# Performance work log

Measured on AMD Instinct MI355X. Metric: run time of the kernel, lower is better.

The kernel has to match this reference:

```python
import jax, jax.numpy as jnp
import numpy as np

D_IN, D_K, D_V = 768, 128, 768


def setup_inputs() -> dict:
    key = jax.random.key(0)
    ks = jax.random.split(key, 7)
    x = jax.random.normal(ks[0], (4, 2048, D_IN), dtype=jnp.float32)
    s_in = 1.0 / np.sqrt(D_IN)
    Wq = jax.random.uniform(ks[1], (D_IN, D_K), minval=-s_in, maxval=s_in, dtype=jnp.float32)
    bq = jax.random.uniform(ks[2], (D_K,), minval=-s_in, maxval=s_in, dtype=jnp.float32)
    Wk = jax.random.uniform(ks[3], (D_IN, D_K), minval=-s_in, maxval=s_in, dtype=jnp.float32)
    bk = jax.random.uniform(ks[4], (D_K,), minval=-s_in, maxval=s_in, dtype=jnp.float32)
    Wv = jax.random.uniform(ks[5], (D_IN, D_V), minval=-s_in, maxval=s_in, dtype=jnp.float32)
    bv = jax.random.uniform(ks[6], (D_V,), minval=-s_in, maxval=s_in, dtype=jnp.float32)
    return {"x": x, "Wq": Wq, "bq": bq, "Wk": Wk, "bk": bk, "Wv": Wv, "bv": bv}


def reference(x, Wq, bq, Wk, bk, Wv, bv):
    # q,k: [b,t,d_k]; v: [b,t,d_v]
    q = jnp.einsum('bti,ik->btk', x, Wq) + bq
    k = jnp.einsum('bti,ik->btk', x, Wk) + bk
    v = jnp.einsum('bti,iv->btv', x, Wv) + bv
    scale = 1.0 / jnp.sqrt(jnp.asarray(D_K, dtype=jnp.float32))
    scores = jnp.einsum('bqk,btk->bqt', q, k) * scale  # [b,t,t]
    attn = jax.nn.softmax(scores, axis=-1)
    return jnp.einsum('bqt,btv->bqv', attn, v)
```

## Files before the change

kernel.cpp:

```cpp
#include <hip/hip_runtime.h>
#include <stdint.h>

typedef unsigned short u16;
typedef __attribute__((ext_vector_type(8))) short short8;
typedef __attribute__((ext_vector_type(4))) float f32x4;

#define BATCH 4
#define SEQ   2048
#define DIN   768
#define DK    128
#define DV    768
#define MTOT  (BATCH*SEQ)
#define NQKV  1024

__device__ __forceinline__ u16 f2bf(float f) {
  union { float f; uint32_t u; } v; v.f = f;
  uint32_t r = v.u + 0x7FFFu + ((v.u >> 16) & 1u);
  return (u16)(r >> 16);
}

template<int N> __device__ __forceinline__ void wait_vmcnt() {
  if constexpr (N == 0) asm volatile("s_waitcnt vmcnt(0)" ::: "memory");
  else if constexpr (N == 5) asm volatile("s_waitcnt vmcnt(5)" ::: "memory");
  else if constexpr (N == 6) asm volatile("s_waitcnt vmcnt(6)" ::: "memory");
}

#define GLOAD_LDS(SRC, DST) \
  __builtin_amdgcn_global_load_lds( \
      (const __attribute__((address_space(1))) unsigned int*)(SRC), \
      (__attribute__((address_space(3))) unsigned int*)(DST), 16, 0, 0)

__global__ __launch_bounds__(256) void prep(
    const float* __restrict__ x, u16* __restrict__ xb,
    const float* __restrict__ Wq, const float* __restrict__ bq,
    const float* __restrict__ Wk, const float* __restrict__ bk,
    const float* __restrict__ Wv, const float* __restrict__ bv,
    u16* __restrict__ WbT, float* __restrict__ biasP) {
  const float qs = 0.088388347648318447f;
  __shared__ u16 tile[64][72];
  int b = blockIdx.x;
  int tid = threadIdx.x;
  if (b < 6144) {
    int i = (b * 256 + tid) * 4;
    float4 v = *(const float4*)(x + i);
    u16 o[4] = { f2bf(v.x), f2bf(v.y), f2bf(v.z), f2bf(v.w) };
    *(uint2*)(xb + i) = *(const uint2*)o;
    return;
  }
  int bid2 = b - 6144;
  int y   = bid2 / 12;
  int i0  = (bid2 - y * 12) * 64;
  const float* W; u16* dst; int ldw, nb; float sc;
  if (y < 2)      { W = Wq; dst = WbT;                      ldw = DK; sc = qs;   nb = y;     }
  else if (y < 4) { W = Wk; dst = WbT + (size_t)DK * DIN;   ldw = DK; sc = 1.0f; nb = y - 2; }
  else            { W = Wv; dst = WbT + (size_t)2*DK * DIN; ldw = DV; sc = 1.0f; nb = y - 4; }
  int n0 = nb * 64;
  if (i0 == 0 && y == 0) {
    for (int n = tid; n < NQKV; n += 256)
      biasP[n] = (n < DK) ? bq[n] * qs : (n < 2*DK ? bk[n - DK] : bv[n - 2*DK]);
  }
  int tr = tid >> 2;
  int tc = (tid & 3) * 16;
  const float* src = W + (size_t)(i0 + tr) * ldw + n0 + tc;
  u16 o[16];
#pragma unroll
  for (int u = 0; u < 16; u += 4) {
    float4 v = *(const float4*)(src + u);
    o[u] = f2bf(v.x * sc); o[u+1] = f2bf(v.y * sc); o[u+2] = f2bf(v.z * sc); o[u+3] = f2bf(v.w * sc);
  }
  *(uint4*)&tile[tr][tc]     = *(const uint4*)&o[0];
  *(uint4*)&tile[tr][tc + 8] = *(const uint4*)&o[8];
  __syncthreads();
  u16 tmp[16];
#pragma unroll
  for (int u = 0; u < 16; ++u) tmp[u] = tile[tc + u][tr];
  u16* d = dst + (size_t)(n0 + tr) * DIN + i0 + tc;
  *(uint4*)d       = *(const uint4*)&tmp[0];
  *(uint4*)(d + 8) = *(const uint4*)&tmp[8];
}

__global__ __launch_bounds__(512, 2) void gemm_proj(
    const u16* __restrict__ A, const u16* __restrict__ BT,
    u16* __restrict__ C0, u16* __restrict__ C1,
    const float* __restrict__ bias)
{
  const int NT = DIN / 64;
  __shared__ u16 As[3][128][64];
  __shared__ u16 Bs[3][256][64];
  const int tid = threadIdx.x;
  const int l   = tid & 63;
  const int wid = tid >> 6;
  const int wm  = wid >> 2;
  const int wn  = wid & 3;

  const int nwg = gridDim.x;
  const int cpx = nwg >> 3;
  const int bid = blockIdx.x;
  const int wg  = (bid & 7) * cpx + (bid >> 3);
  const int by  = wg >> 6;
  const int bx  = wg & 63;
  const int m0  = bx * 128;
  const int n0  = by * 256;

  f32x4 acc[4][4] = {};
  const int lr = l >> 3;
  const int lc = ((l & 7) ^ lr) * 8;

  auto STAGE = [&](int buf, int k0, int i0r, int i1r) {
#pragma unroll
    for (int i = 0; i < 6; ++i) {
      if (i < i0r || i >= i1r) continue;
      int c = wid * 6 + i;
      if (c < 16) {
        GLOAD_LDS(A + (size_t)(m0 + c * 8 + lr) * DIN + k0 + lc, &As[buf][c * 8][0]);
      } else {
        int cb = c - 16;
        GLOAD_LDS(BT + (size_t)(n0 + cb * 8 + lr) * DIN + k0 + lc, &Bs[buf][cb * 8][0]);
      }
    }
  };

  STAGE(0, 0, 0, 6);
  STAGE(1, 64, 0, 6);
  int cur = 0;
  for (int t = 0; t < NT; ++t) {
    if (t == NT - 1) wait_vmcnt<0>(); else wait_vmcnt<6>();
    __builtin_amdgcn_s_barrier();
    const int nxt2 = (cur + 2 >= 3) ? cur - 1 : cur + 2;
    const bool pf = (t + 2 < NT);
#pragma unroll
    for (int ks = 0; ks < 2; ++ks) {
      short8 af[4], bg[4];
#pragma unroll
      for (int i = 0; i < 4; ++i) {
        int row  = wm * 64 + i * 16 + (l & 15);
        int slot = (ks * 4 + (l >> 4)) ^ (row & 7);
        af[i] = *(const short8*)&As[cur][row][slot * 8];
      }
#pragma unroll
      for (int j = 0; j < 4; ++j) {
        int row  = wn * 64 + j * 16 + (l & 15);
        int slot = (ks * 4 + (l >> 4)) ^ (row & 7);
        bg[j] = *(const short8*)&Bs[cur][row][slot * 8];
      }
      if (pf) {
        if (ks == 0) STAGE(nxt2, (t + 2) * 64, 0, 3);
        else         STAGE(nxt2, (t + 2) * 64, 3, 6);
      }
      __builtin_amdgcn_s_setprio(1);
#pragma unroll
      for (int i = 0; i < 4; ++i)
#pragma unroll
        for (int j = 0; j < 4; ++j)
          acc[i][j] = __builtin_amdgcn_mfma_f32_16x16x32_bf16(af[i], bg[j], acc[i][j], 0, 0, 0);
      __builtin_amdgcn_s_setprio(0);
    }
    cur = (cur + 1 == 3) ? 0 : cur + 1;
  }

  const int rbase = (l >> 4) * 4;
  const int cl    = l & 15;
#pragma unroll
  for (int i = 0; i < 4; ++i) {
#pragma unroll
    for (int j = 0; j < 4; ++j) {
      int col  = n0 + wn * 64 + j * 16 + cl;
      int row0 = m0 + wm * 64 + i * 16 + rbase;
      float bv_ = bias[col];
      if (by == 0) {
#pragma unroll
        for (int q = 0; q < 4; ++q)
          C0[(size_t)(row0 + q) * 256 + col] = f2bf(acc[i][j][q] + bv_);
      } else {
        int b = row0 >> 11, t = row0 & 2047;
        u16 o[4];
#pragma unroll
        for (int q = 0; q < 4; ++q) o[q] = f2bf(acc[i][j][q] + bv_);
        *(uint2*)&C1[((size_t)b * DV + (col - 256)) * SEQ + t] = *(const uint2*)o;
      }
    }
  }
}

__global__ __launch_bounds__(512, 2) void sgemm_exp(
    const u16* __restrict__ qk, u16* __restrict__ P)
{
  __shared__ u16 As[256][128];
  __shared__ u16 Bs[256][128];
  const int tid = threadIdx.x;
  const int l   = tid & 63;
  const int wid = tid >> 6;
  const int wm  = wid >> 2;
  const int wn  = wid & 3;

  const int nwg = gridDim.x;
  const int cpx = nwg >> 3;
  const int bid = blockIdx.x;
  const int wg  = (bid & 7) * cpx + (bid >> 3);
  const int z   = wg >> 6;
  const int rem = wg & 63;
  const int by  = rem >> 3;
  const int bx  = rem & 7;
  const int m0  = bx * 256;
  const int n0  = by * 256;

  const u16* A  = qk + (size_t)z * SEQ * 256;
  const u16* BT = qk + DK + (size_t)z * SEQ * 256;

  const int rin = l >> 4;
  const int s16 = l & 15;
#pragma unroll
  for (int i = 0; i < 16; ++i) {
    int c = wid * 16 + i;
    if (c < 64) {
      int r = c * 4 + rin;
      int gs = s16 ^ (r & 7);
      GLOAD_LDS(A + (size_t)(m0 + r) * 256 + gs * 8, &As[c * 4][0]);
    } else {
      int cb = c - 64;
      int r = cb * 4 + rin;
      int gs = s16 ^ (r & 7);
      GLOAD_LDS(BT + (size_t)(n0 + r) * 256 + gs * 8, &Bs[cb * 4][0]);
    }
  }
  __syncthreads();

  f32x4 acc[8][4] = {};
#pragma unroll
  for (int ks = 0; ks < 4; ++ks) {
    short8 af[8], bg[4];
#pragma unroll
    for (int i = 0; i < 8; ++i) {
      int row  = wm * 128 + i * 16 + (l & 15);
      int slot = (ks * 4 + (l >> 4)) ^ (row & 7);
      af[i] = *(const short8*)&As[row][slot * 8];
    }
#pragma unroll
    for (int j = 0; j < 4; ++j) {
      int row  = wn * 64 + j * 16 + (l & 15);
      int slot = (ks * 4 + (l >> 4)) ^ (row & 7);
      bg[j] = *(const short8*)&Bs[row][slot * 8];
    }
#pragma unroll
    for (int i = 0; i < 8; ++i)
#pragma unroll
      for (int j = 0; j < 4; ++j)
        acc[i][j] = __builtin_amdgcn_mfma_f32_16x16x32_bf16(af[i], bg[j], acc[i][j], 0, 0, 0);
  }

  const int rbase = (l >> 4) * 4;
  const int cl    = l & 15;
  u16* Pz = P + (size_t)z * SEQ * SEQ;
#pragma unroll
  for (int i = 0; i < 8; ++i)
#pragma unroll
    for (int j = 0; j < 4; ++j) {
      int col  = n0 + wn * 64 + j * 16 + cl;
      int row0 = m0 + wm * 128 + i * 16 + rbase;
#pragma unroll
      for (int q = 0; q < 4; ++q)
        Pz[(size_t)(row0 + q) * SEQ + col] = f2bf(__expf(acc[i][j][q]));
    }
}

__global__ __launch_bounds__(512, 2) void gemm_pv(
    const u16* __restrict__ P, const u16* __restrict__ vT,
    float* __restrict__ out)
{
  const int NJ = 3, CH = 5, gx = 16, gy = 4, NT = SEQ / 64;
  __shared__ u16 As[3][128][64];
  __shared__ u16 Bs[3][NJ * 64][64];
  const int tid = threadIdx.x;
  const int l   = tid & 63;
  const int wid = tid >> 6;
  const int wm  = wid >> 2;
  const int wn  = wid & 3;

  const int nwg = gridDim.x;
  const int cpx = nwg >> 3;
  const int bid = blockIdx.x;
  const int wg  = (bid & 7) * cpx + (bid >> 3);
  const int z   = wg / (gx * gy);
  const int rem = wg - z * gx * gy;
  const int by  = rem / gx;
  const int bx  = rem - by * gx;
  const int m0  = bx * 128;
  const int n0  = by * (NJ * 64);

  const u16* A  = P  + (size_t)z * SEQ * SEQ;
  const u16* BT = vT + (size_t)z * DV * SEQ;

  f32x4 acc[4][NJ] = {};
  f32x4 accO[4] = {};
  const short8 kOnes = {16256,16256,16256,16256,16256,16256,16256,16256};

  const int lr = l >> 3;
  const int lc = ((l & 7) ^ lr) * 8;
  const int ca = wid * CH;

  auto STAGE = [&](int buf, int k0, int i0, int i1) {
#pragma unroll
    for (int i = 0; i < CH; ++i) {
      if (i < i0 || i >= i1) continue;
      int c = ca + i;
      if (c < 16) {
        GLOAD_LDS(A + (size_t)(m0 + c * 8 + lr) * SEQ + k0 + lc, &As[buf][c * 8][0]);
      } else {
        int cb = c - 16;
        GLOAD_LDS(BT + (size_t)(n0 + cb * 8 + lr) * SEQ + k0 + lc, &Bs[buf][cb * 8][0]);
      }
    }
  };

  STAGE(0, 0, 0, CH);
  STAGE(1, 64, 0, CH);
  int cur = 0;
  for (int t = 0; t < NT; ++t) {
    if (t == NT - 1) wait_vmcnt<0>(); else wait_vmcnt<CH>();
    __builtin_amdgcn_s_barrier();
    const int nxt2 = (cur + 2 >= 3) ? cur - 1 : cur + 2;
    const bool pf = (t + 2 < NT);
#pragma unroll
    for (int ks = 0; ks < 2; ++ks) {
      short8 af[4], bg[NJ];
#pragma unroll
      for (int i = 0; i < 4; ++i) {
        int row  = wm * 64 + i * 16 + (l & 15);
        int slot = (ks * 4 + (l >> 4)) ^ (row & 7);
        af[i] = *(const short8*)&As[cur][row][slot * 8];
      }
#pragma unroll
      for (int j = 0; j < NJ; ++j) {
        int row  = wn * (NJ * 16) + j * 16 + (l & 15);
        int slot = (ks * 4 + (l >> 4)) ^ (row & 7);
        bg[j] = *(const short8*)&Bs[cur][row][slot * 8];
      }
      if (pf) {
        if (ks == 0) STAGE(nxt2, (t + 2) * 64, 0, 3);
        else         STAGE(nxt2, (t + 2) * 64, 3, CH);
      }
      __builtin_amdgcn_s_setprio(1);
#pragma unroll
      for (int i = 0; i < 4; ++i) {
#pragma unroll
        for (int j = 0; j < NJ; ++j)
          acc[i][j] = __builtin_amdgcn_mfma_f32_16x16x32_bf16(af[i], bg[j], acc[i][j], 0, 0, 0);
        accO[i] = __builtin_amdgcn_mfma_f32_16x16x32_bf16(af[i], kOnes, accO[i], 0, 0, 0);
      }
      __builtin_amdgcn_s_setprio(0);
    }
    cur = (cur + 1 == 3) ? 0 : cur + 1;
  }

  const int rbase = (l >> 4) * 4;
  const int cl    = l & 15;
#pragma unroll
  for (int i = 0; i < 4; ++i) {
    int row0 = m0 + wm * 64 + i * 16 + rbase;
    f32x4 rs;
#pragma unroll
    for (int q = 0; q < 4; ++q) rs[q] = 1.0f / accO[i][q];
#pragma unroll
    for (int j = 0; j < NJ; ++j) {
      int col = n0 + wn * (NJ * 16) + j * 16 + cl;
#pragma unroll
      for (int q = 0; q < 4; ++q)
        out[(size_t)z * SEQ * DV + (size_t)(row0 + q) * DV + col] = acc[i][j][q] * rs[q];
    }
  }
}

extern "C" void kernel_launch(void* const* d_in, const int* in_sizes, int n_in,
                              void* d_out, int out_size, void* d_ws, size_t ws_size,
                              hipStream_t stream) {
  const float* x  = (const float*)d_in[0];
  const float* Wq = (const float*)d_in[1];
  const float* bq = (const float*)d_in[2];
  const float* Wk = (const float*)d_in[3];
  const float* bk = (const float*)d_in[4];
  const float* Wv = (const float*)d_in[5];
  const float* bv = (const float*)d_in[6];
  float* out = (float*)d_out;

  size_t off = 0;
  auto alloc = [&](size_t bytes) -> void* {
    void* p = (char*)d_ws + off;
    off += (bytes + 255) & ~(size_t)255;
    return p;
  };
  u16*   xb    = (u16*)alloc((size_t)MTOT * DIN * 2);
  u16*   WbT   = (u16*)alloc((size_t)NQKV * DIN * 2);
  float* biasP = (float*)alloc(NQKV * 4);
  u16*   qk    = (u16*)alloc((size_t)MTOT * 256 * 2);
  u16*   vT    = (u16*)alloc((size_t)BATCH * DV * SEQ * 2);
  u16*   P     = (u16*)alloc((size_t)BATCH * SEQ * SEQ * 2);
  if (off > ws_size) return;

  prep<<<dim3(6144 + 192), dim3(256), 0, stream>>>(x, xb, Wq, bq, Wk, bk, Wv, bv, WbT, biasP);

  gemm_proj<<<dim3(64 * 4), dim3(512), 0, stream>>>(xb, WbT, qk, vT, biasP);

  sgemm_exp<<<dim3(8 * 8 * BATCH), dim3(512), 0, stream>>>(qk, P);

  gemm_pv<<<dim3(16 * 4 * BATCH), dim3(512), 0, stream>>>(P, vT, out);
}
```

Before: 83.19 us.

## Store P in MFMA fragment-tiled layout and load A operands directly to registers

```diff
diff --git a/kernel.cpp b/kernel.cpp
--- a/kernel.cpp
+++ b/kernel.cpp
@@ -21,6 +21,7 @@
 
 template<int N> __device__ __forceinline__ void wait_vmcnt() {
   if constexpr (N == 0) asm volatile("s_waitcnt vmcnt(0)" ::: "memory");
+  else if constexpr (N == 3) asm volatile("s_waitcnt vmcnt(3)" ::: "memory");
   else if constexpr (N == 5) asm volatile("s_waitcnt vmcnt(5)" ::: "memory");
   else if constexpr (N == 6) asm volatile("s_waitcnt vmcnt(6)" ::: "memory");
 }
@@ -183,7 +184,7 @@
 }
 
 __global__ __launch_bounds__(512, 2) void sgemm_exp(
-    const u16* __restrict__ qk, u16* __restrict__ P)
+    const u16* __restrict__ qk, u16* __restrict__ Pt)
 {
   __shared__ u16 As[256][128];
   __shared__ u16 Bs[256][128];
@@ -248,28 +249,40 @@
         acc[i][j] = __builtin_amdgcn_mfma_f32_16x16x32_bf16(af[i], bg[j], acc[i][j], 0, 0, 0);
   }
 
-  const int rbase = (l >> 4) * 4;
-  const int cl    = l & 15;
-  u16* Pz = P + (size_t)z * SEQ * SEQ;
+  __syncthreads();
+  u16* region = (wid < 4) ? (&As[0][0] + wid * 8192) : (&Bs[0][0] + (wid - 4) * 8192);
 #pragma unroll
   for (int i = 0; i < 8; ++i)
 #pragma unroll
-    for (int j = 0; j < 4; ++j) {
-      int col  = n0 + wn * 64 + j * 16 + cl;
-      int row0 = m0 + wm * 128 + i * 16 + rbase;
-#pragma unroll
-      for (int q = 0; q < 4; ++q)
-        Pz[(size_t)(row0 + q) * SEQ + col] = f2bf(__expf(acc[i][j][q]));
+    for (int j = 0; j < 4; ++j)
+#pragma unroll
+      for (int q = 0; q < 4; ++q) {
+        int lq  = i * 16 + (l >> 4) * 4 + q;
+        int lt  = j * 16 + (l & 15);
+        int col = (((lt >> 3) ^ (lq & 7)) << 3) | (lt & 7);
+        region[lq * 64 + col] = f2bf(__expf(acc[i][j][q]));
+      }
+  __syncthreads();
+  u16* Pz = (u16*)Pt + (size_t)z * SEQ * SEQ;
+#pragma unroll
+  for (int i = 0; i < 8; ++i)
+#pragma unroll
+    for (int jj = 0; jj < 2; ++jj) {
+      int lq   = i * 16 + (l & 15);
+      int slot = (jj * 4 + (l >> 4)) ^ (lq & 7);
+      uint4 v  = *(const uint4*)&region[lq * 64 + slot * 8];
+      int gq16 = (m0 >> 4) + wm * 8 + i;
+      int gt32 = (n0 >> 5) + wn * 2 + jj;
+      *(uint4*)&Pz[((size_t)(gq16 * 64 + gt32) * 64 + l) * 8] = v;
     }
 }
 
 __global__ __launch_bounds__(512, 2) void gemm_pv(
-    const u16* __restrict__ P, const u16* __restrict__ vT,
+    const u16* __restrict__ Pt, const u16* __restrict__ vT,
     float* __restrict__ out)
 {
-  const int NJ = 3, CH = 5, gx = 16, gy = 4, NT = SEQ / 64;
-  __shared__ u16 As[3][128][64];
-  __shared__ u16 Bs[3][NJ * 64][64];
+  const int NT = SEQ / 64;
+  __shared__ u16 Bs[3][192][64];
   const int tid = threadIdx.x;
   const int l   = tid & 63;
   const int wid = tid >> 6;
@@ -280,76 +293,79 @@
   const int cpx = nwg >> 3;
   const int bid = blockIdx.x;
   const int wg  = (bid & 7) * cpx + (bid >> 3);
-  const int z   = wg / (gx * gy);
-  const int rem = wg - z * gx * gy;
-  const int by  = rem / gx;
-  const int bx  = rem - by * gx;
+  const int z   = wg >> 6;
+  const int rem = wg & 63;
+  const int by  = rem / 16;
+  const int bx  = rem & 15;
   const int m0  = bx * 128;
-  const int n0  = by * (NJ * 64);
-
-  const u16* A  = P  + (size_t)z * SEQ * SEQ;
-  const u16* BT = vT + (size_t)z * DV * SEQ;
-
-  f32x4 acc[4][NJ] = {};
+  const int n0  = by * 192;
+
+  const u16* Ptz = Pt + (size_t)z * SEQ * SEQ;
+  const u16* BT  = vT + (size_t)z * DV * SEQ;
+
+  f32x4 acc[4][3] = {};
   f32x4 accO[4] = {};
   const short8 kOnes = {16256,16256,16256,16256,16256,16256,16256,16256};
 
   const int lr = l >> 3;
   const int lc = ((l & 7) ^ lr) * 8;
-  const int ca = wid * CH;
-
-  auto STAGE = [&](int buf, int k0, int i0, int i1) {
-#pragma unroll
-    for (int i = 0; i < CH; ++i) {
-      if (i < i0 || i >= i1) continue;
-      int c = ca + i;
-      if (c < 16) {
-        GLOAD_LDS(A + (size_t)(m0 + c * 8 + lr) * SEQ + k0 + lc, &As[buf][c * 8][0]);
-      } else {
-        int cb = c - 16;
-        GLOAD_LDS(BT + (size_t)(n0 + cb * 8 + lr) * SEQ + k0 + lc, &Bs[buf][cb * 8][0]);
-      }
+
+  auto STAGE_B = [&](int buf, int t0) {
+#pragma unroll
+    for (int i = 0; i < 3; ++i) {
+      int c = wid * 3 + i;
+      GLOAD_LDS(BT + (size_t)(n0 + c * 8 + lr) * SEQ + t0 * 64 + lc, &Bs[buf][c * 8][0]);
     }
   };
 
-  STAGE(0, 0, 0, CH);
-  STAGE(1, 64, 0, CH);
-  int cur = 0;
-  for (int t = 0; t < NT; ++t) {
-    if (t == NT - 1) wait_vmcnt<0>(); else wait_vmcnt<CH>();
+  uint4 afA[4][2], afB[4][2];
+  auto AFLOAD = [&](uint4 (&dst)[4][2], int t) {
+#pragma unroll
+    for (int i = 0; i < 4; ++i)
+#pragma unroll
+      for (int ks = 0; ks < 2; ++ks) {
+        const u16* p = Ptz + ((size_t)((bx * 8 + wm * 4 + i) * 64 + (2 * t + ks)) * 64 + l) * 8;
+        asm volatile("global_load_dwordx4 %0, %1, off"
+                     : "=v"(dst[i][ks]) : "v"(p) : "memory");
+      }
+  };
+
+  auto BODY = [&](uint4 (&af)[4][2], uint4 (&afn)[4][2], int t) {
+    if (t == NT - 1) wait_vmcnt<0>(); else wait_vmcnt<3>();
+    __builtin_amdgcn_sched_barrier(0);
     __builtin_amdgcn_s_barrier();
-    const int nxt2 = (cur + 2 >= 3) ? cur - 1 : cur + 2;
-    const bool pf = (t + 2 < NT);
+    if (t + 1 < NT) AFLOAD(afn, t + 1);
+    const int buf = t % 3;
 #pragma unroll
     for (int ks = 0; ks < 2; ++ks) {
-      short8 af[4], bg[NJ];
+      short8 bg[3];
+#pragma unroll
+      for (int j = 0; j < 3; ++j) {
+        int row  = wn * 48 + j * 16 + (l & 15);
+        int slot = (ks * 4 + (l >> 4)) ^ (row & 7);
+        bg[j] = *(const short8*)&Bs[buf][row][slot * 8];
+      }
+      __builtin_amdgcn_s_setprio(1);
 #pragma unroll
       for (int i = 0; i < 4; ++i) {
-        int row  = wm * 64 + i * 16 + (l & 15);
-        int slot = (ks * 4 + (l >> 4)) ^ (row & 7);
-        af[i] = *(const short8*)&As[cur][row][slot * 8];
-      }
-#pragma unroll
-      for (int j = 0; j < NJ; ++j) {
-        int row  = wn * (NJ * 16) + j * 16 + (l & 15);
-        int slot = (ks * 4 + (l >> 4)) ^ (row & 7);
-        bg[j] = *(const short8*)&Bs[cur][row][slot * 8];
-      }
-      if (pf) {
-        if (ks == 0) STAGE(nxt2, (t + 2) * 64, 0, 3);
-        else         STAGE(nxt2, (t + 2) * 64, 3, CH);
-      }
-      __builtin_amdgcn_s_setprio(1);
-#pragma unroll
-      for (int i = 0; i < 4; ++i) {
-#pragma unroll
-        for (int j = 0; j < NJ; ++j)
-          acc[i][j] = __builtin_amdgcn_mfma_f32_16x16x32_bf16(af[i], bg[j], acc[i][j], 0, 0, 0);
-        accO[i] = __builtin_amdgcn_mfma_f32_16x16x32_bf16(af[i], kOnes, accO[i], 0, 0, 0);
+        short8 a = *(const short8*)&af[i][ks];
+#pragma unroll
+        for (int j = 0; j < 3; ++j)
+          acc[i][j] = __builtin_amdgcn_mfma_f32_16x16x32_bf16(a, bg[j], acc[i][j], 0, 0, 0);
+        accO[i] = __builtin_amdgcn_mfma_f32_16x16x32_bf16(a, kOnes, accO[i], 0, 0, 0);
       }
       __builtin_amdgcn_s_setprio(0);
     }
-    cur = (cur + 1 == 3) ? 0 : cur + 1;
+    if (t + 2 < NT) STAGE_B((t + 2) % 3, t + 2);
+    __builtin_amdgcn_s_barrier();
+  };
+
+  AFLOAD(afA, 0);
+  STAGE_B(0, 0);
+  STAGE_B(1, 1);
+  for (int t = 0; t < NT; t += 2) {
+    BODY(afA, afB, t);
+    BODY(afB, afA, t + 1);
   }
 
   const int rbase = (l >> 4) * 4;
@@ -361,8 +377,8 @@
 #pragma unroll
     for (int q = 0; q < 4; ++q) rs[q] = 1.0f / accO[i][q];
 #pragma unroll
-    for (int j = 0; j < NJ; ++j) {
-      int col = n0 + wn * (NJ * 16) + j * 16 + cl;
+    for (int j = 0; j < 3; ++j) {
+      int col = n0 + wn * 48 + j * 16 + cl;
 #pragma unroll
       for (int q = 0; q < 4; ++q)
         out[(size_t)z * SEQ * DV + (size_t)(row0 + q) * DV + col] = acc[i][j][q] * rs[q];
@@ -393,14 +409,14 @@
   float* biasP = (float*)alloc(NQKV * 4);
   u16*   qk    = (u16*)alloc((size_t)MTOT * 256 * 2);
   u16*   vT    = (u16*)alloc((size_t)BATCH * DV * SEQ * 2);
-  u16*   P     = (u16*)alloc((size_t)BATCH * SEQ * SEQ * 2);
+  u16*   Pt    = (u16*)alloc((size_t)BATCH * SEQ * SEQ * 2);
   if (off > ws_size) return;
 
   prep<<<dim3(6144 + 192), dim3(256), 0, stream>>>(x, xb, Wq, bq, Wk, bk, Wv, bv, WbT, biasP);
 
   gemm_proj<<<dim3(64 * 4), dim3(512), 0, stream>>>(xb, WbT, qk, vT, biasP);
 
-  sgemm_exp<<<dim3(8 * 8 * BATCH), dim3(512), 0, stream>>>(qk, P);
-
-  gemm_pv<<<dim3(16 * 4 * BATCH), dim3(512), 0, stream>>>(P, vT, out);
-}
+  sgemm_exp<<<dim3(8 * 8 * BATCH), dim3(512), 0, stream>>>(qk, Pt);
+
+  gemm_pv<<<dim3(16 * 4 * BATCH), dim3(512), 0, stream>>>(Pt, vT, out);
+}
```

Result: no change. 82.43 us (-0.9%).
